# Performance work log

Measured on AMD Instinct MI355X. Metric: run time of the kernel, lower is better.

## Reference

```python
import jax, jax.numpy as jnp
import numpy as np

DIM = 256

def setup_inputs() -> dict:
    key = jax.random.key(0)
    ks = jax.random.split(key, 7)
    B, S, D = 8, 4096, DIM
    scale = 1.0 / np.sqrt(D)
    x = jax.random.normal(ks[0], (B, S, D), dtype=jnp.float32)
    # torch Linear: y = x @ W.T + b, W is [out, in]
    Wq = jax.random.normal(ks[1], (D, D), dtype=jnp.float32) * scale
    Wk = jax.random.normal(ks[2], (D, D), dtype=jnp.float32) * scale
    Wv = jax.random.normal(ks[3], (D, D), dtype=jnp.float32) * scale
    bq = jax.random.normal(ks[4], (D,), dtype=jnp.float32) * 0.01
    bk = jax.random.normal(ks[5], (D,), dtype=jnp.float32) * 0.01
    bv = jax.random.normal(ks[6], (D,), dtype=jnp.float32) * 0.01
    return {"x": x, "Wq": Wq, "bq": bq, "Wk": Wk, "bk": bk, "Wv": Wv, "bv": bv}

def reference(x, Wq, bq, Wk, bk, Wv, bv):
    D = x.shape[-1]
    scale = D ** -0.5
    q = jnp.einsum('bsd,ed->bse', x, Wq) + bq  # [B,S,D]
    k = jnp.einsum('bsd,ed->bse', x, Wk) + bk
    v = jnp.einsum('bsd,ed->bse', x, Wv) + bv
    attn = jnp.einsum('bqd,bkd->bqk', q, k) * scale  # [B,S,S]
    attn = jax.nn.softmax(attn, axis=-1)
    return x + jnp.einsum('bqk,bkd->bqd', attn, v)
```

## Files before the change

### kernel.cpp

```cpp
#include <hip/hip_runtime.h>
#include <hip/hip_bf16.h>

typedef __attribute__((ext_vector_type(8))) short bf16x8;
typedef __attribute__((ext_vector_type(4))) float f32x4;
typedef __attribute__((ext_vector_type(16))) float f32x16;

#define MFMA16(a, b, c) __builtin_amdgcn_mfma_f32_16x16x32_bf16(a, b, c, 0, 0, 0)
#define MFMA32(a, b, c) __builtin_amdgcn_mfma_f32_32x32x16_bf16(a, b, c, 0, 0, 0)

__device__ __forceinline__ short f2bf(float f) {
    union { __hip_bfloat16 h; short s; } u;
    u.h = __float2bfloat16(f);
    return u.s;
}

__device__ __forceinline__ bf16x8 cvt8(const float* __restrict__ p) {
    f32x4 a = *reinterpret_cast<const f32x4*>(p);
    f32x4 b = *reinterpret_cast<const f32x4*>(p + 4);
    bf16x8 r;
    r[0] = f2bf(a[0]); r[1] = f2bf(a[1]); r[2] = f2bf(a[2]); r[3] = f2bf(a[3]);
    r[4] = f2bf(b[0]); r[5] = f2bf(b[1]); r[6] = f2bf(b[2]); r[7] = f2bf(b[3]);
    return r;
}

typedef __attribute__((address_space(1))) const unsigned int g_u32;
typedef __attribute__((address_space(3))) unsigned int l_u32;
__device__ __forceinline__ void gld16(const void* g, void* l) {
    __builtin_amdgcn_global_load_lds((g_u32*)(g), (l_u32*)(l), 16, 0, 0);
}

__global__ void wcvt_kernel(const float* __restrict__ Wq, const float* __restrict__ Wk,
                            const float* __restrict__ Wv, short* __restrict__ Wb)
{
    int t = blockIdx.x * 256 + threadIdx.x;
    int idx = t * 8;
    const float* src = idx < 65536 ? Wq + idx
                     : (idx < 131072 ? Wk + (idx - 65536) : Wv + (idx - 131072));
    *reinterpret_cast<bf16x8*>(Wb + idx) = cvt8(src);
}

__global__ __launch_bounds__(256, 2) void qkv_kernel(
    const float* __restrict__ x, const short* __restrict__ Wb,
    const float* __restrict__ bq, const float* __restrict__ bk, const float* __restrict__ bv,
    short* __restrict__ qo, short* __restrict__ ko, short* __restrict__ vto)
{
    const int wave = threadIdx.x >> 6, lane = threadIdx.x & 63;
    const int l31 = lane & 31, h = lane >> 5;
    const int row0 = blockIdx.x * 128;
    const int wrow = row0 + wave * 32;

    bf16x8 af[16];
    const float* __restrict__ xr = x + (size_t)(wrow + l31) * 256 + h * 8;
#pragma unroll
    for (int kc = 0; kc < 16; ++kc) af[kc] = cvt8(xr + kc * 16);

    __shared__ short tile[128][264];

    for (int proj = 0; proj < 3; ++proj) {
        const short* __restrict__ W = Wb + proj * 65536;
        const float* __restrict__ bias = proj == 0 ? bq : (proj == 1 ? bk : bv);

        f32x16 acc[8];
#pragma unroll
        for (int df = 0; df < 8; ++df)
#pragma unroll
            for (int e = 0; e < 16; ++e) acc[df][e] = 0.f;

#pragma unroll
        for (int kc = 0; kc < 16; ++kc)
#pragma unroll
            for (int df = 0; df < 8; ++df) {
                bf16x8 bfr = *reinterpret_cast<const bf16x8*>(
                    W + (df * 32 + l31) * 256 + kc * 16 + h * 8);
                acc[df] = MFMA32(af[kc], bfr, acc[df]);
            }

        if (proj < 2) {
            short* __restrict__ dst = proj == 0 ? qo : ko;
#pragma unroll
            for (int df = 0; df < 8; ++df) {
                int col = df * 32 + l31;
                float bv_ = bias[col];
#pragma unroll
                for (int rg = 0; rg < 16; ++rg) {
                    int r = (rg & 3) + 8 * (rg >> 2) + 4 * h;
                    dst[(size_t)(wrow + r) * 256 + col] = f2bf(acc[df][rg] + bv_);
                }
            }
        } else {
#pragma unroll
            for (int df = 0; df < 8; ++df) {
                int col = df * 32 + l31;
                float bv_ = bias[col];
#pragma unroll
                for (int rg = 0; rg < 16; ++rg) {
                    int r = (rg & 3) + 8 * (rg >> 2) + 4 * h;
                    tile[wave * 32 + r][col] = f2bf(acc[df][rg] + bv_);
                }
            }
            __syncthreads();
            int d = threadIdx.x;
            int bb = row0 >> 12, s0 = row0 & 4095;
            short* __restrict__ dst = vto + ((size_t)bb * 256 + d) * 4096 + s0;
#pragma unroll
            for (int i = 0; i < 16; ++i) {
                bf16x8 v;
#pragma unroll
                for (int j = 0; j < 8; ++j) v[j] = tile[i * 8 + j][d];
                *reinterpret_cast<bf16x8*>(dst + i * 8) = v;
            }
        }
    }
}

__global__ __launch_bounds__(512, 2) void attn_kernel(
    const short* __restrict__ q, const short* __restrict__ k,
    const short* __restrict__ vt, const float* __restrict__ x,
    float* __restrict__ out)
{
    const int id = blockIdx.x;
    const int b = id & 7, qt = id >> 3;
    const int tid = threadIdx.x;
    const int wave = tid >> 6, lane = tid & 63;
    const int l15 = lane & 15, l4 = lane >> 4;
    const int qg = wave & 3, hh = wave >> 2;
    const int qrow0 = qt * 128 + qg * 32;

    const short* __restrict__ qb = q  + (size_t)b * 4096 * 256;
    const short* __restrict__ kb = k  + (size_t)b * 4096 * 256;
    const short* __restrict__ vb = vt + (size_t)b * 256 * 4096;

    __shared__ short smem[65536];
    __shared__ short plds[8][2][16][40];
    short (*pw)[16][40] = plds[wave];

    bf16x8 qf[2][8];
#pragma unroll
    for (int rg = 0; rg < 2; ++rg) {
        const short* __restrict__ qr =
            qb + (size_t)(qrow0 + rg * 16 + l15) * 256 + l4 * 8;
#pragma unroll
        for (int kc = 0; kc < 8; ++kc)
            qf[rg][kc] = *reinterpret_cast<const bf16x8*>(qr + kc * 32);
    }

    f32x4 o[2][16];
#pragma unroll
    for (int rg = 0; rg < 2; ++rg)
#pragma unroll
        for (int df = 0; df < 16; ++df) { f32x4 z = {0.f,0.f,0.f,0.f}; o[rg][df] = z; }

    float ls[2][4];
#pragma unroll
    for (int rg = 0; rg < 2; ++rg)
#pragma unroll
        for (int r = 0; r < 4; ++r) ls[rg][r] = 0.f;

    const float cs = 0.0625f * 1.44269504f;

#define STAGE(T, B)                                                            \
  { _Pragma("unroll")                                                          \
    for (int i = 0; i < 8; ++i) {                                              \
        int c = i * 512 + tid;                                                 \
        const short* src;                                                      \
        if (c < 2048) {                                                        \
            int hh_ = c >> 10, nf = (c >> 9) & 1, kc = (c >> 6) & 7, l = c & 63;\
            src = kb + (size_t)((T) * 64 + hh_ * 32 + nf * 16 + (l & 15)) * 256\
                     + kc * 32 + (l >> 4) * 8;                                 \
        } else {                                                               \
            int s = c & 2047;                                                  \
            int hh_ = s >> 10, df = (s >> 6) & 15, l = s & 63;                 \
            src = vb + (size_t)(df * 16 + (l & 15)) * 4096 + (T) * 64          \
                     + hh_ * 32 + (l >> 4) * 8;                                \
        }                                                                      \
        gld16(src, &smem[((B) * 4096 + c) * 8]);                               \
    } }

    STAGE(0, 0);
    __syncthreads();

    for (int t = 0; t < 64; ++t) {
        const int buf = t & 1;
        if (t < 63) STAGE(t + 1, buf ^ 1);

        const short* __restrict__ kbase = smem + ((size_t)buf * 4096 + hh * 1024) * 8;
        const short* __restrict__ vbase = smem + ((size_t)buf * 4096 + 2048 + hh * 1024) * 8;

        f32x4 sacc[2][2];
#pragma unroll
        for (int rg = 0; rg < 2; ++rg)
#pragma unroll
            for (int nf = 0; nf < 2; ++nf) { f32x4 z = {0.f,0.f,0.f,0.f}; sacc[rg][nf] = z; }
#pragma unroll
        for (int nf = 0; nf < 2; ++nf)
#pragma unroll
            for (int kc = 0; kc < 8; ++kc) {
                bf16x8 kf = *reinterpret_cast<const bf16x8*>(
                    kbase + (nf * 512 + kc * 64 + lane) * 8);
                sacc[0][nf] = MFMA16(qf[0][kc], kf, sacc[0][nf]);
                sacc[1][nf] = MFMA16(qf[1][kc], kf, sacc[1][nf]);
            }

#pragma unroll
        for (int rg = 0; rg < 2; ++rg)
#pragma unroll
            for (int nf = 0; nf < 2; ++nf)
#pragma unroll
                for (int r = 0; r < 4; ++r) {
                    float p = exp2f(sacc[rg][nf][r] * cs);
                    ls[rg][r] += p;
                    pw[rg][l4 * 4 + r][nf * 16 + l15] = f2bf(p);
                }
        bf16x8 pf0 = *reinterpret_cast<const bf16x8*>(&pw[0][l15][l4 * 8]);
        bf16x8 pf1 = *reinterpret_cast<const bf16x8*>(&pw[1][l15][l4 * 8]);

#pragma unroll
        for (int df = 0; df < 16; ++df) {
            bf16x8 vf = *reinterpret_cast<const bf16x8*>(
                vbase + (df * 64 + lane) * 8);
            o[0][df] = MFMA16(pf0, vf, o[0][df]);
            o[1][df] = MFMA16(pf1, vf, o[1][df]);
        }

        __syncthreads();
    }

#pragma unroll
    for (int rg = 0; rg < 2; ++rg)
#pragma unroll
        for (int r = 0; r < 4; ++r) {
            float v = ls[rg][r];
#pragma unroll
            for (int d = 1; d < 16; d <<= 1) v += __shfl_xor(v, d);
            ls[rg][r] = v;
        }

    f32x4* __restrict__ fo = (f32x4*)smem;
    float* __restrict__ fl = (float*)plds;

    __syncthreads();

    if (hh == 1) {
#pragma unroll
        for (int rg = 0; rg < 2; ++rg) {
#pragma unroll
            for (int df = 0; df < 16; ++df)
                fo[((qg * 2 + rg) * 16 + df) * 64 + lane] = o[rg][df];
#pragma unroll
            for (int r = 0; r < 4; ++r)
                fl[((qg * 2 + rg) * 4 + r) * 64 + lane] = ls[rg][r];
        }
    }
    __syncthreads();

    if (hh == 0) {
#pragma unroll
        for (int rg = 0; rg < 2; ++rg) {
            float inv[4];
#pragma unroll
            for (int r = 0; r < 4; ++r)
                inv[r] = 1.0f / (ls[rg][r] + fl[((qg * 2 + rg) * 4 + r) * 64 + lane]);
#pragma unroll
            for (int df = 0; df < 16; ++df) {
                f32x4 od = fo[((qg * 2 + rg) * 16 + df) * 64 + lane];
                int col = df * 16 + l15;
#pragma unroll
                for (int r = 0; r < 4; ++r) {
                    size_t row = (size_t)b * 4096 + qrow0 + rg * 16 + l4 * 4 + r;
                    out[row * 256 + col] =
                        (o[rg][df][r] + od[r]) * inv[r] + x[row * 256 + col];
                }
            }
        }
    }
#undef STAGE
}

extern "C" void kernel_launch(void* const* d_in, const int* in_sizes, int n_in,
                              void* d_out, int out_size, void* d_ws, size_t ws_size,
                              hipStream_t stream) {
    const float* x  = (const float*)d_in[0];
    const float* Wq = (const float*)d_in[1];
    const float* bq = (const float*)d_in[2];
    const float* Wk = (const float*)d_in[3];
    const float* bk = (const float*)d_in[4];
    const float* Wv = (const float*)d_in[5];
    const float* bv = (const float*)d_in[6];
    float* out = (float*)d_out;

    char* ws = (char*)d_ws;
    short* qb  = (short*)ws;
    short* kb  = (short*)(ws + (size_t)16 * 1024 * 1024);
    short* vtb = (short*)(ws + (size_t)32 * 1024 * 1024);
    short* Wb  = (short*)d_out;

    wcvt_kernel<<<96, 256, 0, stream>>>(Wq, Wk, Wv, Wb);

    qkv_kernel<<<256, 256, 0, stream>>>(x, Wb, bq, bk, bv, qb, kb, vtb);

    attn_kernel<<<256, 512, 0, stream>>>(qb, kb, vtb, x, out);
}
```

Before: 339.4 us.

## Unroll attention pipeline into ping-pong buffers with explicit waitcnt and repack W layout

The attention loop is unrolled by two over separate LDS buffers A and B. Each step uses an explicit s_waitcnt vmcnt(0) plus s_barrier and a sched_barrier in place of __syncthreads, so buffer addressing becomes static and the compiler's conservative waits are avoided. Separately, the bf16 weight conversion now writes W in a fragment-major layout, so the qkv kernel's MFMA B-operand loads become contiguous across lanes instead of 512-byte strided. The risk is that the sched_barriers stop the compiler from interleaving instructions across stages, and the manual waits must stay correct.

```diff
diff --git a/kernel.cpp b/kernel.cpp
--- a/kernel.cpp
+++ b/kernel.cpp
@@ -29,14 +29,20 @@
     __builtin_amdgcn_global_load_lds((g_u32*)(g), (l_u32*)(l), 16, 0, 0);
 }
 
+#define SBAR()    asm volatile("s_barrier" ::: "memory")
+#define VMCNT(N)  asm volatile("s_waitcnt vmcnt(" #N ")" ::: "memory")
+
 __global__ void wcvt_kernel(const float* __restrict__ Wq, const float* __restrict__ Wk,
                             const float* __restrict__ Wv, short* __restrict__ Wb)
 {
     int t = blockIdx.x * 256 + threadIdx.x;
-    int idx = t * 8;
-    const float* src = idx < 65536 ? Wq + idx
-                     : (idx < 131072 ? Wk + (idx - 65536) : Wv + (idx - 131072));
-    *reinterpret_cast<bf16x8*>(Wb + idx) = cvt8(src);
+    int out_row = t & 255;
+    int h  = (t >> 8) & 1;
+    int kc = (t >> 9) & 15;
+    int proj = t >> 13;
+    const float* src = (proj == 0 ? Wq : (proj == 1 ? Wk : Wv))
+                     + out_row * 256 + kc * 16 + h * 8;
+    *reinterpret_cast<bf16x8*>(Wb + t * 8) = cvt8(src);
 }
 
 __global__ __launch_bounds__(256, 2) void qkv_kernel(
@@ -71,7 +77,7 @@
 #pragma unroll
             for (int df = 0; df < 8; ++df) {
                 bf16x8 bfr = *reinterpret_cast<const bf16x8*>(
-                    W + (df * 32 + l31) * 256 + kc * 16 + h * 8);
+                    W + ((kc * 2 + h) * 256 + df * 32 + l31) * 8);
                 acc[df] = MFMA32(af[kc], bfr, acc[df]);
             }
 
@@ -130,7 +136,8 @@
     const short* __restrict__ kb = k  + (size_t)b * 4096 * 256;
     const short* __restrict__ vb = vt + (size_t)b * 256 * 4096;
 
-    __shared__ short smem[65536];
+    __shared__ short smemA[32768];
+    __shared__ short smemB[32768];
     __shared__ short plds[8][2][16][40];
     short (*pw)[16][40] = plds[wave];
 
@@ -158,7 +165,7 @@
 
     const float cs = 0.0625f * 1.44269504f;
 
-#define STAGE(T, B)                                                            \
+#define STAGE(T, BUF)                                                          \
   { _Pragma("unroll")                                                          \
     for (int i = 0; i < 8; ++i) {                                              \
         int c = i * 512 + tid;                                                 \
@@ -173,56 +180,69 @@
             src = vb + (size_t)(df * 16 + (l & 15)) * 4096 + (T) * 64          \
                      + hh_ * 32 + (l >> 4) * 8;                                \
         }                                                                      \
-        gld16(src, &smem[((B) * 4096 + c) * 8]);                               \
+        gld16(src, &BUF[c * 8]);                                               \
     } }
 
-    STAGE(0, 0);
-    __syncthreads();
-
-    for (int t = 0; t < 64; ++t) {
-        const int buf = t & 1;
-        if (t < 63) STAGE(t + 1, buf ^ 1);
-
-        const short* __restrict__ kbase = smem + ((size_t)buf * 4096 + hh * 1024) * 8;
-        const short* __restrict__ vbase = smem + ((size_t)buf * 4096 + 2048 + hh * 1024) * 8;
-
-        f32x4 sacc[2][2];
-#pragma unroll
-        for (int rg = 0; rg < 2; ++rg)
-#pragma unroll
-            for (int nf = 0; nf < 2; ++nf) { f32x4 z = {0.f,0.f,0.f,0.f}; sacc[rg][nf] = z; }
-#pragma unroll
-        for (int nf = 0; nf < 2; ++nf)
-#pragma unroll
-            for (int kc = 0; kc < 8; ++kc) {
-                bf16x8 kf = *reinterpret_cast<const bf16x8*>(
-                    kbase + (nf * 512 + kc * 64 + lane) * 8);
-                sacc[0][nf] = MFMA16(qf[0][kc], kf, sacc[0][nf]);
-                sacc[1][nf] = MFMA16(qf[1][kc], kf, sacc[1][nf]);
-            }
-
-#pragma unroll
-        for (int rg = 0; rg < 2; ++rg)
-#pragma unroll
-            for (int nf = 0; nf < 2; ++nf)
-#pragma unroll
-                for (int r = 0; r < 4; ++r) {
-                    float p = exp2f(sacc[rg][nf][r] * cs);
-                    ls[rg][r] += p;
-                    pw[rg][l4 * 4 + r][nf * 16 + l15] = f2bf(p);
-                }
-        bf16x8 pf0 = *reinterpret_cast<const bf16x8*>(&pw[0][l15][l4 * 8]);
-        bf16x8 pf1 = *reinterpret_cast<const bf16x8*>(&pw[1][l15][l4 * 8]);
-
-#pragma unroll
-        for (int df = 0; df < 16; ++df) {
-            bf16x8 vf = *reinterpret_cast<const bf16x8*>(
-                vbase + (df * 64 + lane) * 8);
-            o[0][df] = MFMA16(pf0, vf, o[0][df]);
-            o[1][df] = MFMA16(pf1, vf, o[1][df]);
-        }
-
-        __syncthreads();
+#define COMPUTE(BUF)                                                           \
+  {                                                                            \
+    const short* __restrict__ kbase = BUF + (hh * 1024) * 8;                   \
+    const short* __restrict__ vbase = BUF + (2048 + hh * 1024) * 8;            \
+    f32x4 sacc[2][2];                                                          \
+    _Pragma("unroll")                                                          \
+    for (int rg = 0; rg < 2; ++rg)                                             \
+        _Pragma("unroll")                                                      \
+        for (int nf = 0; nf < 2; ++nf) {                                       \
+            f32x4 z = {0.f,0.f,0.f,0.f}; sacc[rg][nf] = z;                     \
+        }                                                                      \
+    _Pragma("unroll")                                                          \
+    for (int nf = 0; nf < 2; ++nf)                                             \
+        _Pragma("unroll")                                                      \
+        for (int kc = 0; kc < 8; ++kc) {                                       \
+            bf16x8 kf = *reinterpret_cast<const bf16x8*>(                      \
+                kbase + (nf * 512 + kc * 64 + lane) * 8);                      \
+            sacc[0][nf] = MFMA16(qf[0][kc], kf, sacc[0][nf]);                  \
+            sacc[1][nf] = MFMA16(qf[1][kc], kf, sacc[1][nf]);                  \
+        }                                                                      \
+    _Pragma("unroll")                                                          \
+    for (int rg = 0; rg < 2; ++rg)                                             \
+        _Pragma("unroll")                                                      \
+        for (int nf = 0; nf < 2; ++nf)                                         \
+            _Pragma("unroll")                                                  \
+            for (int r = 0; r < 4; ++r) {                                      \
+                float p = exp2f(sacc[rg][nf][r] * cs);                         \
+                ls[rg][r] += p;                                                \
+                pw[rg][l4 * 4 + r][nf * 16 + l15] = f2bf(p);                   \
+            }                                                                  \
+    bf16x8 pf0 = *reinterpret_cast<const bf16x8*>(&pw[0][l15][l4 * 8]);        \
+    bf16x8 pf1 = *reinterpret_cast<const bf16x8*>(&pw[1][l15][l4 * 8]);        \
+    _Pragma("unroll")                                                          \
+    for (int df = 0; df < 16; ++df) {                                          \
+        bf16x8 vf = *reinterpret_cast<const bf16x8*>(                          \
+            vbase + (df * 64 + lane) * 8);                                     \
+        o[0][df] = MFMA16(pf0, vf, o[0][df]);                                  \
+        o[1][df] = MFMA16(pf1, vf, o[1][df]);                                  \
+    }                                                                          \
+  }
+
+    STAGE(0, smemA);
+    VMCNT(0);
+    SBAR();
+    __builtin_amdgcn_sched_barrier(0);
+
+    for (int tt = 0; tt < 32; ++tt) {
+        const int t1 = 2 * tt + 1;
+
+        STAGE(2 * tt + 1, smemB);
+        COMPUTE(smemA);
+        VMCNT(0);
+        SBAR();
+        __builtin_amdgcn_sched_barrier(0);
+
+        if (t1 < 63) STAGE(t1 + 1, smemA);
+        COMPUTE(smemB);
+        if (t1 < 63) VMCNT(0);
+        SBAR();
+        __builtin_amdgcn_sched_barrier(0);
     }
 
 #pragma unroll
@@ -235,21 +255,23 @@
             ls[rg][r] = v;
         }
 
-    f32x4* __restrict__ fo = (f32x4*)smem;
-    float* __restrict__ fl = (float*)plds;
+    f32x4* __restrict__ foA = (f32x4*)smemA;
+    f32x4* __restrict__ foB = (f32x4*)smemB;
+    float* __restrict__ fl  = (float*)plds;
 
     __syncthreads();
 
     if (hh == 1) {
 #pragma unroll
-        for (int rg = 0; rg < 2; ++rg) {
-#pragma unroll
-            for (int df = 0; df < 16; ++df)
-                fo[((qg * 2 + rg) * 16 + df) * 64 + lane] = o[rg][df];
+        for (int df = 0; df < 16; ++df) {
+            foA[(qg * 16 + df) * 64 + lane] = o[0][df];
+            foB[(qg * 16 + df) * 64 + lane] = o[1][df];
+        }
+#pragma unroll
+        for (int rg = 0; rg < 2; ++rg)
 #pragma unroll
             for (int r = 0; r < 4; ++r)
                 fl[((qg * 2 + rg) * 4 + r) * 64 + lane] = ls[rg][r];
-        }
     }
     __syncthreads();
 
@@ -262,7 +284,7 @@
                 inv[r] = 1.0f / (ls[rg][r] + fl[((qg * 2 + rg) * 4 + r) * 64 + lane]);
 #pragma unroll
             for (int df = 0; df < 16; ++df) {
-                f32x4 od = fo[((qg * 2 + rg) * 16 + df) * 64 + lane];
+                f32x4 od = (rg == 0 ? foA : foB)[(qg * 16 + df) * 64 + lane];
                 int col = df * 16 + l15;
 #pragma unroll
                 for (int r = 0; r < 4; ++r) {
@@ -274,6 +296,7 @@
         }
     }
 #undef STAGE
+#undef COMPUTE
 }
 
 extern "C" void kernel_launch(void* const* d_in, const int* in_sizes, int n_in,
```

Measured after the change: 577.8 us. 70.3% more time.
